# Kernel tuning notes

Measured on AMD Instinct MI355X. Metric: run time of the kernel, lower is better.

## Reference

```python
import jax, jax.numpy as jnp
import numpy as np

H = 8  # num_heads
EPS = 1e-5


def layer_norm(x, g, b):
    mu = jnp.mean(x, axis=-1, keepdims=True)
    var = jnp.mean((x - mu) ** 2, axis=-1, keepdims=True)
    return (x - mu) * jax.lax.rsqrt(var + EPS) * g + b


def setup_inputs() -> dict:
    key = jax.random.key(0)
    ks = jax.random.split(key, 8)
    B, N, C = 2, 2048, 512
    Dff = 2048
    s = 0.02
    x = jax.random.normal(ks[0], (B, N, C), dtype=jnp.float32)
    mask = (jax.random.uniform(ks[1], (N, N)) > 0.5).astype(jnp.float32)
    return {
        "x": x,
        "mask": mask,
        "w_qkv": jax.random.normal(ks[2], (3 * C, C), dtype=jnp.float32) * s,
        "w_proj": jax.random.normal(ks[3], (C, C), dtype=jnp.float32) * s,
        "b_proj": jnp.zeros((C,), jnp.float32),
        "g1": jnp.ones((C,), jnp.float32),
        "beta1": jnp.zeros((C,), jnp.float32),
        "g2": jnp.ones((C,), jnp.float32),
        "beta2": jnp.zeros((C,), jnp.float32),
        "w1": jax.random.normal(ks[4], (Dff, C), dtype=jnp.float32) * s,
        "bm1": jnp.zeros((Dff,), jnp.float32),
        "w2": jax.random.normal(ks[5], (C, Dff), dtype=jnp.float32) * s,
        "bm2": jnp.zeros((C,), jnp.float32),
    }


def attn_block(h, mask, w_qkv, w_proj, b_proj):
    B, N, C = h.shape
    hd = C // H
    scale = hd ** -0.5
    qkv = (h @ w_qkv.T).reshape(B, N, 3, H, hd)
    q, k, v = jnp.moveaxis(qkv, 2, 0)          # each [B, N, H, hd]
    q = q.transpose(0, 2, 1, 3)                 # [B, H, N, hd]
    k = k.transpose(0, 2, 1, 3)
    v = v.transpose(0, 2, 1, 3)
    attn = jnp.einsum("bhnd,bhmd->bhnm", q, k) * scale
    attn = attn * mask                          # multiplicative sparse mask
    attn = jax.nn.softmax(attn, axis=-1)
    o = jnp.einsum("bhnm,bhmd->bhnd", attn, v)
    o = o.transpose(0, 2, 1, 3).reshape(B, N, C)
    return o @ w_proj.T + b_proj


def reference(x, mask, w_qkv, w_proj, b_proj, g1, beta1, g2, beta2, w1, bm1, w2, bm2):
    # pre-norm transformer block, dropout/drop_path disabled (eval)
    y = x + attn_block(layer_norm(x, g1, beta1), mask, w_qkv, w_proj, b_proj)
    h = layer_norm(y, g2, beta2)
    h = jax.nn.gelu(h @ w1.T + bm1, approximate=False)  # torch F.gelu default (erf)
    z = y + (h @ w2.T + bm2)
    return z
```

## Files before the change

kernel.cpp:

```cpp
#include <hip/hip_runtime.h>
#include <cmath>
#include <stdint.h>

#define N_SEQ 2048
#define C_DIM 512
#define BATCH 2
#define NHEAD 8
#define DFF   2048
#define M_ROWS (BATCH * N_SEQ)

typedef unsigned short ushort_t;
typedef __bf16 bf16x8 __attribute__((ext_vector_type(8)));
typedef float  f32x4  __attribute__((ext_vector_type(4)));

__device__ __forceinline__ float bf2f(ushort_t u) {
    union { unsigned int i; float f; } v; v.i = ((unsigned int)u) << 16; return v.f;
}
__device__ __forceinline__ ushort_t f2bf_(float f) {
    union { float f; unsigned int i; } v; v.f = f;
    unsigned int r = v.i + 0x7fffu + ((v.i >> 16) & 1u);
    return (ushort_t)(r >> 16);
}

__device__ __forceinline__ void load_lds16(const ushort_t* g, ushort_t* lds_wave_base) {
    __builtin_amdgcn_global_load_lds(
        (const __attribute__((address_space(1))) void*)g,
        (__attribute__((address_space(3))) void*)lds_wave_base, 16, 0, 0);
}

__global__ void probe_kernel(const unsigned int* __restrict__ g1w, int* __restrict__ flag) {
    if (threadIdx.x == 0 && blockIdx.x == 0)
        *flag = (g1w[0] == 0x3F800000u) ? 1 : 0;
}

__global__ __launch_bounds__(256) void convert_kernel(const int* __restrict__ flag,
        const void* w_qkv, const void* w_proj, const void* w1, const void* w2,
        ushort_t* wq_bf, ushort_t* wp_bf, ushort_t* w1_bf, ushort_t* w2_bf) {
    long e = ((long)blockIdx.x * 256 + threadIdx.x) * 8;
    const void* src; ushort_t* dst; long off;
    if      (e < 786432)  { src = w_qkv; dst = wq_bf;  off = e; }
    else if (e < 1048576) { src = w_proj; dst = wp_bf; off = e - 786432; }
    else if (e < 2097152) { src = w1;    dst = w1_bf;  off = e - 1048576; }
    else                  { src = w2;    dst = w2_bf;  off = e - 2097152; }
    bf16x8 r;
    if (*flag) {
        const float4* q = (const float4*)((const float*)src + off);
        float4 a = q[0], b = q[1];
        r[0]=(__bf16)a.x; r[1]=(__bf16)a.y; r[2]=(__bf16)a.z; r[3]=(__bf16)a.w;
        r[4]=(__bf16)b.x; r[5]=(__bf16)b.y; r[6]=(__bf16)b.z; r[7]=(__bf16)b.w;
    } else {
        r = *(const bf16x8*)((const ushort_t*)src + off);
    }
    *(bf16x8*)(dst + off) = r;
}

template <typename TX, typename TG>
__device__ __forceinline__ void ln_body(const TX* __restrict__ x, const TG* __restrict__ g,
                                        const TG* __restrict__ b, ushort_t* __restrict__ out) {
    int row  = blockIdx.x * 4 + (threadIdx.x >> 6);
    int lane = threadIdx.x & 63;
    const TX* xr = x + (size_t)row * C_DIM + lane * 8;
    float v[8];
    if (sizeof(TX) == 2) {
        bf16x8 t = *(const bf16x8*)xr;
        #pragma unroll
        for (int j = 0; j < 8; ++j) v[j] = (float)t[j];
    } else {
        const float4* q = (const float4*)xr;
        float4 a = q[0], c = q[1];
        v[0]=a.x; v[1]=a.y; v[2]=a.z; v[3]=a.w; v[4]=c.x; v[5]=c.y; v[6]=c.z; v[7]=c.w;
    }
    float s = 0.f, sq = 0.f;
    #pragma unroll
    for (int j = 0; j < 8; ++j) { s += v[j]; sq += v[j] * v[j]; }
    #pragma unroll
    for (int m = 1; m < 64; m <<= 1) { s += __shfl_xor(s, m, 64); sq += __shfl_xor(sq, m, 64); }
    float mean = s * (1.0f / C_DIM);
    float var  = fmaxf(sq * (1.0f / C_DIM) - mean * mean, 0.0f);
    float rs = rsqrtf(var + 1e-5f);
    float gv[8], bv[8];
    const TG* gp = g + lane * 8; const TG* bp = b + lane * 8;
    if (sizeof(TG) == 2) {
        bf16x8 tg = *(const bf16x8*)gp, tb = *(const bf16x8*)bp;
        #pragma unroll
        for (int j = 0; j < 8; ++j) { gv[j] = (float)tg[j]; bv[j] = (float)tb[j]; }
    } else {
        const float4* qg = (const float4*)gp; const float4* qb = (const float4*)bp;
        float4 a=qg[0], c=qg[1], d=qb[0], e=qb[1];
        gv[0]=a.x;gv[1]=a.y;gv[2]=a.z;gv[3]=a.w;gv[4]=c.x;gv[5]=c.y;gv[6]=c.z;gv[7]=c.w;
        bv[0]=d.x;bv[1]=d.y;bv[2]=d.z;bv[3]=d.w;bv[4]=e.x;bv[5]=e.y;bv[6]=e.z;bv[7]=e.w;
    }
    bf16x8 o;
    #pragma unroll
    for (int j = 0; j < 8; ++j) o[j] = (__bf16)((v[j] - mean) * rs * gv[j] + bv[j]);
    *(bf16x8*)(out + (size_t)row * C_DIM + lane * 8) = o;
}

__global__ __launch_bounds__(256) void ln1_kernel(const int* __restrict__ flag, const void* x,
                                                  const void* g, const void* b, ushort_t* out) {
    if (*flag) ln_body<float, float>((const float*)x, (const float*)g, (const float*)b, out);
    else       ln_body<ushort_t, ushort_t>((const ushort_t*)x, (const ushort_t*)g, (const ushort_t*)b, out);
}
__global__ __launch_bounds__(256) void ln2_kernel(const int* __restrict__ flag, const ushort_t* y,
                                                  const void* g, const void* b, ushort_t* out) {
    if (*flag) ln_body<ushort_t, float>(y, (const float*)g, (const float*)b, out);
    else       ln_body<ushort_t, ushort_t>(y, (const ushort_t*)g, (const ushort_t*)b, out);
}

template <int K, int WN, bool HAS_BIAS, int ACT, int RES_MODE, int OUT_MODE>
__global__ __launch_bounds__(256) void gemm_kernel(const int* __restrict__ flag,
        const ushort_t* __restrict__ A, const ushort_t* __restrict__ W,
        const void* __restrict__ bias, const void* __restrict__ res,
        void* __restrict__ Cout, int Nout) {
    constexpr int BN = WN * 32;
    __shared__ __align__(16) ushort_t As[128 * 32];
    __shared__ __align__(16) ushort_t Bs[BN * 32];
    int t = threadIdx.x;
    int wave = t >> 6, lane = t & 63, quad = lane >> 4, l16 = lane & 15;
    int wave_m = wave >> 1, wave_n = wave & 1;
    int row0 = blockIdx.y * 128, col0 = blockIdx.x * BN;

    f32x4 acc[4][WN] = {};
    int arow = t >> 2, kofs = (t & 3) * 8;

    for (int k0 = 0; k0 < K; k0 += 32) {
        load_lds16(A + (size_t)(row0 + arow) * K + k0 + kofs,      As + wave * 512);
        load_lds16(A + (size_t)(row0 + 64 + arow) * K + k0 + kofs, As + 2048 + wave * 512);
        load_lds16(W + (size_t)(col0 + arow) * K + k0 + kofs,      Bs + wave * 512);
        if (BN == 128)
            load_lds16(W + (size_t)(col0 + 64 + arow) * K + k0 + kofs, Bs + 2048 + wave * 512);
        __syncthreads();
        bf16x8 af[4], bfr[WN];
        #pragma unroll
        for (int i = 0; i < 4; ++i)
            af[i] = *(const bf16x8*)&As[(wave_m * 64 + i * 16 + l16) * 32 + quad * 8];
        #pragma unroll
        for (int j = 0; j < WN; ++j)
            bfr[j] = *(const bf16x8*)&Bs[(wave_n * WN * 16 + j * 16 + l16) * 32 + quad * 8];
        #pragma unroll
        for (int i = 0; i < 4; ++i)
            #pragma unroll
            for (int j = 0; j < WN; ++j)
                acc[i][j] = __builtin_amdgcn_mfma_f32_16x16x32_bf16(af[i], bfr[j], acc[i][j], 0, 0, 0);
        __syncthreads();
    }

    int is32 = *flag;
    #pragma unroll
    for (int j = 0; j < WN; ++j) {
        int col = col0 + wave_n * WN * 16 + j * 16 + l16;
        float bv = 0.0f;
        if (HAS_BIAS) bv = is32 ? ((const float*)bias)[col] : bf2f(((const ushort_t*)bias)[col]);
        #pragma unroll
        for (int i = 0; i < 4; ++i) {
            #pragma unroll
            for (int r = 0; r < 4; ++r) {
                int row = row0 + wave_m * 64 + i * 16 + quad * 4 + r;
                float v = acc[i][j][r] + bv;
                if (ACT == 1) v = 0.5f * v * (1.0f + erff(v * 0.70710678118654752f));
                size_t idx = (size_t)row * Nout + col;
                if (RES_MODE == 1) v += is32 ? ((const float*)res)[idx] : bf2f(((const ushort_t*)res)[idx]);
                if (RES_MODE == 3) v += bf2f(((const ushort_t*)res)[idx]);
                if (OUT_MODE == 0) ((ushort_t*)Cout)[idx] = f2bf_(v);
                else { if (is32) ((float*)Cout)[idx] = v; else ((ushort_t*)Cout)[idx] = f2bf_(v); }
            }
        }
    }
}

__global__ __launch_bounds__(256, 4) void attn_kernel(const int* __restrict__ flag,
        const ushort_t* __restrict__ qkv, const void* __restrict__ mask,
        ushort_t* __restrict__ Opart, float* __restrict__ Lpart) {
    __shared__ __align__(16) ushort_t Ks[64][68];
    __shared__ __align__(16) ushort_t VTs[64][68];
    __shared__ __align__(16) ushort_t Ps[4][16][68];
    int bh = blockIdx.x, b = bh >> 3, h = bh & 7;
    int sp = blockIdx.z;
    int t = threadIdx.x;
    int wave = t >> 6, lane = t & 63, quad = lane >> 4, l16 = lane & 15;
    int row0 = blockIdx.y * 64 + wave * 16;
    int is32 = *flag;

    const ushort_t* base = qkv + (size_t)b * N_SEQ * 1536;
    const ushort_t* qp = base + h * 64;
    const ushort_t* kp = base + 512 + h * 64;
    const ushort_t* vp = base + 1024 + h * 64;
    const float* mask32 = (const float*)mask;
    const ushort_t* mask16 = (const ushort_t*)mask;

    bf16x8 aq[2];
    #pragma unroll
    for (int c = 0; c < 2; ++c)
        aq[c] = *(const bf16x8*)(qp + (size_t)(row0 + l16) * 1536 + c * 32 + quad * 8);

    f32x4 o_acc[4] = {};
    float lsum[4] = {};
    const float scale = 0.125f;

    int k_key[2], k_d[2], v_key[2], v_db[2];
    #pragma unroll
    for (int s = 0; s < 2; ++s) {
        int e = s * 256 + t;
        k_key[s] = e >> 3;  k_d[s]  = (e & 7) * 8;
        v_key[s] = e & 63;  v_db[s] = (e >> 6) * 8;
    }
    const int n_base = sp * 1024;
    bf16x8 kreg[2], vreg[2];
    #pragma unroll
    for (int s = 0; s < 2; ++s) {
        kreg[s] = *(const bf16x8*)(kp + (size_t)(n_base + k_key[s]) * 1536 + k_d[s]);
        vreg[s] = *(const bf16x8*)(vp + (size_t)(n_base + v_key[s]) * 1536 + v_db[s]);
    }

    for (int i = 0; i < 16; ++i) {
        int n0 = n_base + i * 64;
        __syncthreads();
        #pragma unroll
        for (int s = 0; s < 2; ++s)
            *(bf16x8*)&Ks[k_key[s]][k_d[s]] = kreg[s];
        #pragma unroll
        for (int s = 0; s < 2; ++s)
            #pragma unroll
            for (int j = 0; j < 8; ++j)
                VTs[v_db[s] + j][v_key[s]] = __builtin_bit_cast(unsigned short, vreg[s][j]);
        __syncthreads();
        if (i < 15) {
            int n1 = n0 + 64;
            #pragma unroll
            for (int s = 0; s < 2; ++s) {
                kreg[s] = *(const bf16x8*)(kp + (size_t)(n1 + k_key[s]) * 1536 + k_d[s]);
                vreg[s] = *(const bf16x8*)(vp + (size_t)(n1 + v_key[s]) * 1536 + v_db[s]);
            }
        }
        f32x4 s_acc[4] = {};
        #pragma unroll
        for (int g = 0; g < 4; ++g)
            #pragma unroll
            for (int c = 0; c < 2; ++c) {
                bf16x8 bk = *(const bf16x8*)&Ks[g * 16 + l16][c * 32 + quad * 8];
                s_acc[g] = __builtin_amdgcn_mfma_f32_16x16x32_bf16(aq[c], bk, s_acc[g], 0, 0, 0);
            }
        #pragma unroll
        for (int g = 0; g < 4; ++g)
            #pragma unroll
            for (int r = 0; r < 4; ++r) {
                size_t midx = (size_t)(row0 + quad * 4 + r) * N_SEQ + n0 + g * 16 + l16;
                float m = is32 ? mask32[midx] : bf2f(mask16[midx]);
                float p = __expf(s_acc[g][r] * scale * m);
                lsum[r] += p;
                Ps[wave][quad * 4 + r][g * 16 + l16] = __builtin_bit_cast(unsigned short, (__bf16)p);
            }
        bf16x8 pf[2];
        #pragma unroll
        for (int c = 0; c < 2; ++c)
            pf[c] = *(const bf16x8*)&Ps[wave][l16][c * 32 + quad * 8];
        #pragma unroll
        for (int d = 0; d < 4; ++d)
            #pragma unroll
            for (int c = 0; c < 2; ++c) {
                bf16x8 bv = *(const bf16x8*)&VTs[d * 16 + l16][c * 32 + quad * 8];
                o_acc[d] = __builtin_amdgcn_mfma_f32_16x16x32_bf16(pf[c], bv, o_acc[d], 0, 0, 0);
            }
    }
    #pragma unroll
    for (int m = 1; m < 16; m <<= 1)
        #pragma unroll
        for (int r = 0; r < 4; ++r) lsum[r] += __shfl_xor(lsum[r], m, 64);
    ushort_t* op = Opart + (size_t)(sp * 16 + bh) * N_SEQ * 64;
    #pragma unroll
    for (int r = 0; r < 4; ++r) {
        int row = row0 + quad * 4 + r;
        #pragma unroll
        for (int d = 0; d < 4; ++d)
            op[(size_t)row * 64 + d * 16 + l16] = f2bf_(o_acc[d][r]);
    }
    if (l16 == 0) {
        #pragma unroll
        for (int r = 0; r < 4; ++r)
            Lpart[(size_t)(sp * 16 + bh) * N_SEQ + row0 + quad * 4 + r] = lsum[r];
    }
}

__global__ __launch_bounds__(256) void combine_kernel(const ushort_t* __restrict__ Opart,
        const float* __restrict__ Lpart, ushort_t* __restrict__ attno) {
    int gid = blockIdx.x * 256 + threadIdx.x;
    int rowg = gid >> 4;
    int dq = (gid & 15) * 4;
    int bh = rowg >> 11, q = rowg & 2047, b = bh >> 3, h = bh & 7;
    const size_t SP = (size_t)16 * N_SEQ * 64;
    ushort4 o0 = *(const ushort4*)&Opart[(size_t)rowg * 64 + dq];
    ushort4 o1 = *(const ushort4*)&Opart[SP + (size_t)rowg * 64 + dq];
    float inv = 1.0f / (Lpart[rowg] + Lpart[16 * N_SEQ + rowg]);
    ushort4 res;
    res.x = f2bf_((bf2f(o0.x) + bf2f(o1.x)) * inv);
    res.y = f2bf_((bf2f(o0.y) + bf2f(o1.y)) * inv);
    res.z = f2bf_((bf2f(o0.z) + bf2f(o1.z)) * inv);
    res.w = f2bf_((bf2f(o0.w) + bf2f(o1.w)) * inv);
    *(ushort4*)&attno[((size_t)b * N_SEQ + q) * C_DIM + h * 64 + dq] = res;
}

extern "C" void kernel_launch(void* const* d_in, const int* in_sizes, int n_in,
                              void* d_out, int out_size, void* d_ws, size_t ws_size,
                              hipStream_t stream) {
    char* ws = (char*)d_ws;
    const size_t KB = 1024;
    int*      flag  = (int*)ws;
    ushort_t* wq_bf = (ushort_t*)(ws + 256 * KB);
    ushort_t* wp_bf = (ushort_t*)(ws + 2048 * KB);
    ushort_t* w1_bf = (ushort_t*)(ws + 2560 * KB);
    ushort_t* w2_bf = (ushort_t*)(ws + 4608 * KB);
    ushort_t* qkv   = (ushort_t*)(ws + 6656 * KB);
    ushort_t* Opart = (ushort_t*)(ws + 18944 * KB);
    float*    Lpart = (float*)   (ws + 27648 * KB);
    ushort_t* attno = (ushort_t*)(ws + 27904 * KB);
    ushort_t* y     = (ushort_t*)(ws + 32000 * KB);
    ushort_t* h     = (ushort_t*)(ws + 36096 * KB);
    ushort_t* gmid  = (ushort_t*)(ws + 6656 * KB);

    probe_kernel<<<1, 64, 0, stream>>>((const unsigned int*)d_in[5], flag);
    convert_kernel<<<1536, 256, 0, stream>>>(flag, d_in[2], d_in[3], d_in[9], d_in[11],
                                             wq_bf, wp_bf, w1_bf, w2_bf);
    ln1_kernel<<<M_ROWS / 4, 256, 0, stream>>>(flag, d_in[0], d_in[5], d_in[6], h);
    gemm_kernel<512, 4, false, 0, 0, 0><<<dim3(1536 / 128, 32), 256, 0, stream>>>(
        flag, h, wq_bf, nullptr, nullptr, qkv, 1536);
    attn_kernel<<<dim3(BATCH * NHEAD, N_SEQ / 64, 2), 256, 0, stream>>>(flag, qkv, d_in[1], Opart, Lpart);
    combine_kernel<<<2048, 256, 0, stream>>>(Opart, Lpart, attno);
    gemm_kernel<512, 2, true, 0, 1, 0><<<dim3(C_DIM / 64, 32), 256, 0, stream>>>(
        flag, attno, wp_bf, d_in[4], d_in[0], y, C_DIM);
    ln2_kernel<<<M_ROWS / 4, 256, 0, stream>>>(flag, y, d_in[7], d_in[8], h);
    gemm_kernel<512, 4, true, 1, 0, 0><<<dim3(DFF / 128, 32), 256, 0, stream>>>(
        flag, h, w1_bf, d_in[10], nullptr, gmid, DFF);
    gemm_kernel<2048, 2, true, 0, 3, 2><<<dim3(C_DIM / 64, 32), 256, 0, stream>>>(
        flag, gmid, w2_bf, d_in[12], y, d_out, C_DIM);
}
```

Before: 307.9 us.

## Shrink GEMM tiles, split attention keys four ways, and prefetch mask into registers

GEMM tiles shrink (BN fixed at 64, BM 64 or 128) so the launches use more blocks. The attention key range is now split across 4 blocks instead of 2, each block covering 512 keys, and combine_kernel reduces 4 partials. Mask values for the next key tile are loaded into registers one iteration ahead so their global latency is hidden, and attention launch bounds ask for 5 waves per SIMD. The workspace is reorganized to hold the larger Opart buffer. The costs are extra partial-output traffic and less data reuse in the smaller GEMM tiles.

```diff
diff --git a/kernel.cpp b/kernel.cpp
--- a/kernel.cpp
+++ b/kernel.cpp
@@ -107,55 +107,54 @@
     else       ln_body<ushort_t, ushort_t>(y, (const ushort_t*)g, (const ushort_t*)b, out);
 }
 
-template <int K, int WN, bool HAS_BIAS, int ACT, int RES_MODE, int OUT_MODE>
+template <int BM, int K, bool HAS_BIAS, int ACT, int RES_MODE, int OUT_MODE>
 __global__ __launch_bounds__(256) void gemm_kernel(const int* __restrict__ flag,
         const ushort_t* __restrict__ A, const ushort_t* __restrict__ W,
         const void* __restrict__ bias, const void* __restrict__ res,
         void* __restrict__ Cout, int Nout) {
-    constexpr int BN = WN * 32;
-    __shared__ __align__(16) ushort_t As[128 * 32];
-    __shared__ __align__(16) ushort_t Bs[BN * 32];
+    constexpr int MT = BM / 32;
+    __shared__ __align__(16) ushort_t As[BM * 32];
+    __shared__ __align__(16) ushort_t Bs[64 * 32];
     int t = threadIdx.x;
     int wave = t >> 6, lane = t & 63, quad = lane >> 4, l16 = lane & 15;
     int wave_m = wave >> 1, wave_n = wave & 1;
-    int row0 = blockIdx.y * 128, col0 = blockIdx.x * BN;
-
-    f32x4 acc[4][WN] = {};
+    int row0 = blockIdx.y * BM, col0 = blockIdx.x * 64;
+
+    f32x4 acc[MT][2] = {};
     int arow = t >> 2, kofs = (t & 3) * 8;
 
     for (int k0 = 0; k0 < K; k0 += 32) {
-        load_lds16(A + (size_t)(row0 + arow) * K + k0 + kofs,      As + wave * 512);
-        load_lds16(A + (size_t)(row0 + 64 + arow) * K + k0 + kofs, As + 2048 + wave * 512);
-        load_lds16(W + (size_t)(col0 + arow) * K + k0 + kofs,      Bs + wave * 512);
-        if (BN == 128)
-            load_lds16(W + (size_t)(col0 + 64 + arow) * K + k0 + kofs, Bs + 2048 + wave * 512);
+        load_lds16(A + (size_t)(row0 + arow) * K + k0 + kofs, As + wave * 512);
+        if (BM == 128)
+            load_lds16(A + (size_t)(row0 + 64 + arow) * K + k0 + kofs, As + 2048 + wave * 512);
+        load_lds16(W + (size_t)(col0 + arow) * K + k0 + kofs, Bs + wave * 512);
         __syncthreads();
-        bf16x8 af[4], bfr[WN];
-        #pragma unroll
-        for (int i = 0; i < 4; ++i)
-            af[i] = *(const bf16x8*)&As[(wave_m * 64 + i * 16 + l16) * 32 + quad * 8];
-        #pragma unroll
-        for (int j = 0; j < WN; ++j)
-            bfr[j] = *(const bf16x8*)&Bs[(wave_n * WN * 16 + j * 16 + l16) * 32 + quad * 8];
-        #pragma unroll
-        for (int i = 0; i < 4; ++i)
-            #pragma unroll
-            for (int j = 0; j < WN; ++j)
+        bf16x8 af[MT], bfr[2];
+        #pragma unroll
+        for (int i = 0; i < MT; ++i)
+            af[i] = *(const bf16x8*)&As[(wave_m * (BM / 2) + i * 16 + l16) * 32 + quad * 8];
+        #pragma unroll
+        for (int j = 0; j < 2; ++j)
+            bfr[j] = *(const bf16x8*)&Bs[(wave_n * 32 + j * 16 + l16) * 32 + quad * 8];
+        #pragma unroll
+        for (int i = 0; i < MT; ++i)
+            #pragma unroll
+            for (int j = 0; j < 2; ++j)
                 acc[i][j] = __builtin_amdgcn_mfma_f32_16x16x32_bf16(af[i], bfr[j], acc[i][j], 0, 0, 0);
         __syncthreads();
     }
 
     int is32 = *flag;
     #pragma unroll
-    for (int j = 0; j < WN; ++j) {
-        int col = col0 + wave_n * WN * 16 + j * 16 + l16;
+    for (int j = 0; j < 2; ++j) {
+        int col = col0 + wave_n * 32 + j * 16 + l16;
         float bv = 0.0f;
         if (HAS_BIAS) bv = is32 ? ((const float*)bias)[col] : bf2f(((const ushort_t*)bias)[col]);
         #pragma unroll
-        for (int i = 0; i < 4; ++i) {
+        for (int i = 0; i < MT; ++i) {
             #pragma unroll
             for (int r = 0; r < 4; ++r) {
-                int row = row0 + wave_m * 64 + i * 16 + quad * 4 + r;
+                int row = row0 + wave_m * (BM / 2) + i * 16 + quad * 4 + r;
                 float v = acc[i][j][r] + bv;
                 if (ACT == 1) v = 0.5f * v * (1.0f + erff(v * 0.70710678118654752f));
                 size_t idx = (size_t)row * Nout + col;
@@ -168,7 +167,7 @@
     }
 }
 
-__global__ __launch_bounds__(256, 4) void attn_kernel(const int* __restrict__ flag,
+__global__ __launch_bounds__(256, 5) void attn_kernel(const int* __restrict__ flag,
         const ushort_t* __restrict__ qkv, const void* __restrict__ mask,
         ushort_t* __restrict__ Opart, float* __restrict__ Lpart) {
     __shared__ __align__(16) ushort_t Ks[64][68];
@@ -187,6 +186,9 @@
     const ushort_t* vp = base + 1024 + h * 64;
     const float* mask32 = (const float*)mask;
     const ushort_t* mask16 = (const ushort_t*)mask;
+    size_t mbase[4];
+    #pragma unroll
+    for (int r = 0; r < 4; ++r) mbase[r] = (size_t)(row0 + quad * 4 + r) * N_SEQ;
 
     bf16x8 aq[2];
     #pragma unroll
@@ -204,15 +206,23 @@
         k_key[s] = e >> 3;  k_d[s]  = (e & 7) * 8;
         v_key[s] = e & 63;  v_db[s] = (e >> 6) * 8;
     }
-    const int n_base = sp * 1024;
+    const int n_base = sp * 512;
     bf16x8 kreg[2], vreg[2];
     #pragma unroll
     for (int s = 0; s < 2; ++s) {
         kreg[s] = *(const bf16x8*)(kp + (size_t)(n_base + k_key[s]) * 1536 + k_d[s]);
         vreg[s] = *(const bf16x8*)(vp + (size_t)(n_base + v_key[s]) * 1536 + v_db[s]);
     }
-
-    for (int i = 0; i < 16; ++i) {
+    float mreg[16];
+    #pragma unroll
+    for (int g = 0; g < 4; ++g)
+        #pragma unroll
+        for (int r = 0; r < 4; ++r) {
+            size_t midx = mbase[r] + n_base + g * 16 + l16;
+            mreg[g * 4 + r] = is32 ? mask32[midx] : bf2f(mask16[midx]);
+        }
+
+    for (int i = 0; i < 8; ++i) {
         int n0 = n_base + i * 64;
         __syncthreads();
         #pragma unroll
@@ -224,7 +234,7 @@
             for (int j = 0; j < 8; ++j)
                 VTs[v_db[s] + j][v_key[s]] = __builtin_bit_cast(unsigned short, vreg[s][j]);
         __syncthreads();
-        if (i < 15) {
+        if (i < 7) {
             int n1 = n0 + 64;
             #pragma unroll
             for (int s = 0; s < 2; ++s) {
@@ -244,12 +254,19 @@
         for (int g = 0; g < 4; ++g)
             #pragma unroll
             for (int r = 0; r < 4; ++r) {
-                size_t midx = (size_t)(row0 + quad * 4 + r) * N_SEQ + n0 + g * 16 + l16;
-                float m = is32 ? mask32[midx] : bf2f(mask16[midx]);
-                float p = __expf(s_acc[g][r] * scale * m);
+                float p = __expf(s_acc[g][r] * scale * mreg[g * 4 + r]);
                 lsum[r] += p;
                 Ps[wave][quad * 4 + r][g * 16 + l16] = __builtin_bit_cast(unsigned short, (__bf16)p);
             }
+        if (i < 7) {
+            #pragma unroll
+            for (int g = 0; g < 4; ++g)
+                #pragma unroll
+                for (int r = 0; r < 4; ++r) {
+                    size_t midx = mbase[r] + n0 + 64 + g * 16 + l16;
+                    mreg[g * 4 + r] = is32 ? mask32[midx] : bf2f(mask16[midx]);
+                }
+        }
         bf16x8 pf[2];
         #pragma unroll
         for (int c = 0; c < 2; ++c)
@@ -288,14 +305,18 @@
     int dq = (gid & 15) * 4;
     int bh = rowg >> 11, q = rowg & 2047, b = bh >> 3, h = bh & 7;
     const size_t SP = (size_t)16 * N_SEQ * 64;
-    ushort4 o0 = *(const ushort4*)&Opart[(size_t)rowg * 64 + dq];
-    ushort4 o1 = *(const ushort4*)&Opart[SP + (size_t)rowg * 64 + dq];
-    float inv = 1.0f / (Lpart[rowg] + Lpart[16 * N_SEQ + rowg]);
+    float acc[4] = {};
+    float l = 0.0f;
+    #pragma unroll
+    for (int sp = 0; sp < 4; ++sp) {
+        ushort4 o = *(const ushort4*)&Opart[sp * SP + (size_t)rowg * 64 + dq];
+        acc[0] += bf2f(o.x); acc[1] += bf2f(o.y); acc[2] += bf2f(o.z); acc[3] += bf2f(o.w);
+        l += Lpart[(size_t)sp * 16 * N_SEQ + rowg];
+    }
+    float inv = 1.0f / l;
     ushort4 res;
-    res.x = f2bf_((bf2f(o0.x) + bf2f(o1.x)) * inv);
-    res.y = f2bf_((bf2f(o0.y) + bf2f(o1.y)) * inv);
-    res.z = f2bf_((bf2f(o0.z) + bf2f(o1.z)) * inv);
-    res.w = f2bf_((bf2f(o0.w) + bf2f(o1.w)) * inv);
+    res.x = f2bf_(acc[0] * inv); res.y = f2bf_(acc[1] * inv);
+    res.z = f2bf_(acc[2] * inv); res.w = f2bf_(acc[3] * inv);
     *(ushort4*)&attno[((size_t)b * N_SEQ + q) * C_DIM + h * 64 + dq] = res;
 }
 
@@ -306,30 +327,30 @@
     const size_t KB = 1024;
     int*      flag  = (int*)ws;
     ushort_t* wq_bf = (ushort_t*)(ws + 256 * KB);
-    ushort_t* wp_bf = (ushort_t*)(ws + 2048 * KB);
-    ushort_t* w1_bf = (ushort_t*)(ws + 2560 * KB);
-    ushort_t* w2_bf = (ushort_t*)(ws + 4608 * KB);
-    ushort_t* qkv   = (ushort_t*)(ws + 6656 * KB);
-    ushort_t* Opart = (ushort_t*)(ws + 18944 * KB);
-    float*    Lpart = (float*)   (ws + 27648 * KB);
-    ushort_t* attno = (ushort_t*)(ws + 27904 * KB);
-    ushort_t* y     = (ushort_t*)(ws + 32000 * KB);
-    ushort_t* h     = (ushort_t*)(ws + 36096 * KB);
-    ushort_t* gmid  = (ushort_t*)(ws + 6656 * KB);
+    ushort_t* wp_bf = (ushort_t*)(ws + 1792 * KB);
+    ushort_t* w1_bf = (ushort_t*)(ws + 2304 * KB);
+    ushort_t* w2_bf = (ushort_t*)(ws + 4352 * KB);
+    ushort_t* h     = (ushort_t*)(ws + 6400 * KB);
+    ushort_t* attno = (ushort_t*)(ws + 6400 * KB);
+    ushort_t* qkv   = (ushort_t*)(ws + 10496 * KB);
+    ushort_t* Opart = (ushort_t*)(ws + 22784 * KB);
+    float*    Lpart = (float*)   (ws + 39168 * KB);
+    ushort_t* y     = (ushort_t*)(ws + 35072 * KB);
+    ushort_t* gmid  = (ushort_t*)(ws + 10496 * KB);
 
     probe_kernel<<<1, 64, 0, stream>>>((const unsigned int*)d_in[5], flag);
     convert_kernel<<<1536, 256, 0, stream>>>(flag, d_in[2], d_in[3], d_in[9], d_in[11],
                                              wq_bf, wp_bf, w1_bf, w2_bf);
     ln1_kernel<<<M_ROWS / 4, 256, 0, stream>>>(flag, d_in[0], d_in[5], d_in[6], h);
-    gemm_kernel<512, 4, false, 0, 0, 0><<<dim3(1536 / 128, 32), 256, 0, stream>>>(
+    gemm_kernel<128, 512, false, 0, 0, 0><<<dim3(1536 / 64, 32), 256, 0, stream>>>(
         flag, h, wq_bf, nullptr, nullptr, qkv, 1536);
-    attn_kernel<<<dim3(BATCH * NHEAD, N_SEQ / 64, 2), 256, 0, stream>>>(flag, qkv, d_in[1], Opart, Lpart);
+    attn_kernel<<<dim3(BATCH * NHEAD, N_SEQ / 64, 4), 256, 0, stream>>>(flag, qkv, d_in[1], Opart, Lpart);
     combine_kernel<<<2048, 256, 0, stream>>>(Opart, Lpart, attno);
-    gemm_kernel<512, 2, true, 0, 1, 0><<<dim3(C_DIM / 64, 32), 256, 0, stream>>>(
+    gemm_kernel<64, 512, true, 0, 1, 0><<<dim3(C_DIM / 64, 64), 256, 0, stream>>>(
         flag, attno, wp_bf, d_in[4], d_in[0], y, C_DIM);
     ln2_kernel<<<M_ROWS / 4, 256, 0, stream>>>(flag, y, d_in[7], d_in[8], h);
-    gemm_kernel<512, 4, true, 1, 0, 0><<<dim3(DFF / 128, 32), 256, 0, stream>>>(
+    gemm_kernel<128, 512, true, 1, 0, 0><<<dim3(DFF / 64, 32), 256, 0, stream>>>(
         flag, h, w1_bf, d_in[10], nullptr, gmid, DFF);
-    gemm_kernel<2048, 2, true, 0, 3, 2><<<dim3(C_DIM / 64, 32), 256, 0, stream>>>(
+    gemm_kernel<64, 2048, true, 0, 3, 2><<<dim3(C_DIM / 64, 64), 256, 0, stream>>>(
         flag, gmid, w2_bf, d_in[12], y, d_out, C_DIM);
 }
```

After: 275.9 us. -10.4%, faster.
